# Optimization experiments

Measured on AMD Instinct MI355X. Metric: run time of the kernel, lower is better.

The kernel has to match this reference:

```python
import jax, jax.numpy as jnp
import numpy as np

B, T, F = 64, 96, 32          # batch, window_size, num_features
H_ENC, H_DEC = 128, 128       # encoder / decoder hidden sizes


def _lstm_cell(x, h, c, k, r, b):
    # Keras LSTMCell math: gates ordered i, f, g(candidate), o
    z = x @ k + h @ r + b
    i, f, g, o = jnp.split(z, 4, axis=-1)
    i = jax.nn.sigmoid(i)
    f = jax.nn.sigmoid(f)
    g = jnp.tanh(g)
    o = jax.nn.sigmoid(o)
    c_new = f * c + i * g
    h_new = o * jnp.tanh(c_new)
    return h_new, c_new


def setup_inputs() -> dict:
    key = jax.random.key(0)
    ks = jax.random.split(key, 20)
    s = 0.05
    d = {
        "inputs": jax.random.normal(ks[0], (B, T, F), jnp.float32),
        # encoder LSTMCell (input dim = F)
        "enc_k": jax.random.normal(ks[1], (F, 4 * H_ENC), jnp.float32) * s,
        "enc_r": jax.random.normal(ks[2], (H_ENC, 4 * H_ENC), jnp.float32) * s,
        "enc_b": jnp.zeros((4 * H_ENC,), jnp.float32),
        # encoder attention MLP: in = 2*H_ENC + T -> H_ENC -> 1
        "ae_w1": jax.random.normal(ks[3], (2 * H_ENC + T, H_ENC), jnp.float32) * s,
        "ae_b1": jnp.zeros((H_ENC,), jnp.float32),
        "ae_w2": jax.random.normal(ks[4], (H_ENC, 1), jnp.float32) * s,
        "ae_b2": jnp.zeros((1,), jnp.float32),
        # decoder LSTMCell (input dim = H_DEC, the fc output)
        "dec_k": jax.random.normal(ks[5], (H_DEC, 4 * H_DEC), jnp.float32) * s,
        "dec_r": jax.random.normal(ks[6], (H_DEC, 4 * H_DEC), jnp.float32) * s,
        "dec_b": jnp.zeros((4 * H_DEC,), jnp.float32),
        # decoder attention MLP: in = 2*H_DEC + H_ENC -> H_ENC -> 1
        "ad_w1": jax.random.normal(ks[7], (2 * H_DEC + H_ENC, H_ENC), jnp.float32) * s,
        "ad_b1": jnp.zeros((H_ENC,), jnp.float32),
        "ad_w2": jax.random.normal(ks[8], (H_ENC, 1), jnp.float32) * s,
        "ad_b2": jnp.zeros((1,), jnp.float32),
        # fc: (context H_ENC + y_prev 1) -> H_DEC
        "fc_w": jax.random.normal(ks[9], (H_ENC + 1, H_DEC), jnp.float32) * s,
        "fc_b": jnp.zeros((H_DEC,), jnp.float32),
        # fc_final: (d_n H_DEC + context H_ENC) -> F
        "ff_w": jax.random.normal(ks[10], (H_DEC + H_ENC, F), jnp.float32) * s,
        "ff_b": jnp.zeros((F,), jnp.float32),
    }
    return d


def reference(inputs, enc_k, enc_r, enc_b, ae_w1, ae_b1, ae_w2, ae_b2,
              dec_k, dec_r, dec_b, ad_w1, ad_b1, ad_w2, ad_b2,
              fc_w, fc_b, ff_w, ff_b):
    b, t, f = inputs.shape
    h_enc = enc_r.shape[0]
    h_dec = dec_r.shape[0]
    x_perm = jnp.transpose(inputs, (0, 2, 1))  # [B, F, T] (constant over time)

    # ---------------- encoder: input-attention LSTM over time ----------------
    def enc_step(carry, x_t):
        h, s = carry  # each [B, H_enc]
        hb = jnp.broadcast_to(h[:, None, :], (b, f, h_enc))
        sb = jnp.broadcast_to(s[:, None, :], (b, f, h_enc))
        cat = jnp.concatenate([hb, sb, x_perm], axis=2)       # [B, F, 2H+T]
        e = jnp.tanh(cat @ ae_w1 + ae_b1) @ ae_w2 + ae_b2     # [B, F, 1]
        alpha = jax.nn.softmax(e[..., 0], axis=1)             # [B, F]
        x_tilde = alpha * x_t                                 # [B, F]
        h, s = _lstm_cell(x_tilde, h, s, enc_k, enc_r, enc_b)
        return (h, s), h

    init = (jnp.zeros((b, h_enc), inputs.dtype), jnp.zeros((b, h_enc), inputs.dtype))
    _, h_all = jax.lax.scan(enc_step, init, jnp.transpose(inputs, (1, 0, 2)))
    x_encoded = jnp.transpose(h_all, (1, 0, 2))               # [B, T, H_enc]

    # ---------------- decoder: temporal-attention LSTM over time -------------
    y_prev = inputs[:, :, -1]                                 # [B, T]

    def dec_step(carry, y_t):
        d, c, _ = carry
        db = jnp.broadcast_to(d[:, None, :], (b, t, h_dec))
        cb = jnp.broadcast_to(c[:, None, :], (b, t, h_dec))
        cat = jnp.concatenate([db, cb, x_encoded], axis=2)    # [B, T, 2Hd+He]
        e = jnp.tanh(cat @ ad_w1 + ad_b1) @ ad_w2 + ad_b2     # [B, T, 1]
        beta = jax.nn.softmax(e[..., 0], axis=1)              # [B, T]
        ctx = jnp.einsum("bt,bth->bh", beta, x_encoded)       # [B, H_enc]
        y_tilde = jnp.concatenate([ctx, y_t[:, None]], axis=1) @ fc_w + fc_b
        d, c = _lstm_cell(y_tilde, d, c, dec_k, dec_r, dec_b)
        return (d, c, ctx), None

    init_d = (jnp.zeros((b, h_dec), inputs.dtype),
              jnp.zeros((b, h_dec), inputs.dtype),
              jnp.zeros((b, h_enc), inputs.dtype))
    (d_n, _, ctx), _ = jax.lax.scan(dec_step, init_d, jnp.transpose(y_prev, (1, 0)))

    y_pred = jnp.concatenate([d_n, ctx], axis=1) @ ff_w + ff_b  # [B, F]
    return y_pred[:, None, :]                                   # [B, 1, F]
```

## Files before the change

kernel.cpp:

```cpp
#include <hip/hip_runtime.h>

#define TT 96
#define FF 32
#define HH 128
#define G4 512
#define LOG2E 1.4426950408889634f

typedef _Float16 h2 __attribute__((ext_vector_type(2)));

__device__ __forceinline__ float fexp2(float x){ return __builtin_amdgcn_exp2f(x); }
__device__ __forceinline__ float frcp(float x){ return __builtin_amdgcn_rcpf(x); }
__device__ __forceinline__ float fsigmoid(float x){ return frcp(1.0f + fexp2(-LOG2E*x)); }
__device__ __forceinline__ float ftanh(float x){
    float u = fexp2(2.0f*LOG2E*x);
    return 1.0f - 2.0f*frcp(1.0f + u);
}
__device__ __forceinline__ h2 pk(float a, float b){
    h2 r; r.x = (_Float16)a; r.y = (_Float16)b; return r;
}
__device__ __forceinline__ unsigned pku(float a, float b){
    return __builtin_bit_cast(unsigned, pk(a, b));
}
__device__ __forceinline__ h2 u2h(unsigned v){ return __builtin_bit_cast(h2, v); }
__device__ __forceinline__ float fdot2(h2 a, h2 b, float c){
#if __has_builtin(__builtin_amdgcn_fdot2)
    return __builtin_amdgcn_fdot2(a, b, c, false);
#else
    return c + (float)a.x*(float)b.x + (float)a.y*(float)b.y;
#endif
}

__global__ __launch_bounds__(1024, 1)
void k_enc(const float* __restrict__ inputs,
           const float* __restrict__ enc_k,
           const float* __restrict__ enc_r,
           const float* __restrict__ enc_b,
           const float* __restrict__ ae_w1,
           const float* __restrict__ ae_b1,
           const float* __restrict__ ae_w2,
           const float* __restrict__ ad_w1,
           const float* __restrict__ fc_w,
           const float* __restrict__ fc_b,
           const float* __restrict__ dec_k,
           const float* __restrict__ dec_b,
           h2* __restrict__ Gp,
           float* __restrict__ gy,
           float* __restrict__ gb,
           float* __restrict__ ws_xenc,
           float* __restrict__ ws_xept){
    if (blockIdx.x >= 64){
        int blk = blockIdx.x - 64, tid = threadIdx.x;
        if (tid >= 256) return;
        int u0 = tid, u1 = tid + 256;
        if (blk < 16){
            float a0[8], a1[8];
            #pragma unroll
            for (int r = 0; r < 8; ++r){ a0[r] = 0.f; a1[r] = 0.f; }
            for (int m = 0; m < 128; ++m){
                float d0 = dec_k[m*G4 + u0], d1 = dec_k[m*G4 + u1];
                #pragma unroll
                for (int r = 0; r < 8; ++r){
                    float w = fc_w[(blk*8 + r)*HH + m];
                    a0[r] += w * d0; a1[r] += w * d1;
                }
            }
            #pragma unroll
            for (int c = 0; c < 4; ++c){
                Gp[(blk*G4 + u0)*4 + c] = pk(a0[2*c], a0[2*c+1]);
                Gp[(blk*G4 + u1)*4 + c] = pk(a1[2*c], a1[2*c+1]);
            }
        } else if (blk == 16){
            float a0 = 0.f, a1 = 0.f;
            for (int m = 0; m < 128; ++m){
                float w = fc_w[128*HH + m];
                a0 += w * dec_k[m*G4 + u0]; a1 += w * dec_k[m*G4 + u1];
            }
            gy[u0] = a0; gy[u1] = a1;
        } else {
            float a0 = 0.f, a1 = 0.f;
            for (int m = 0; m < 128; ++m){
                float w = fc_b[m];
                a0 += w * dec_k[m*G4 + u0]; a1 += w * dec_k[m*G4 + u1];
            }
            gb[u0] = a0 + dec_b[u0]; gb[u1] = a1 + dec_b[u1];
        }
        return;
    }

    extern __shared__ float lds[];
    uint4* KLH4 = (uint4*)lds;
    float* XPJT = lds + 8192;
    float* XIN  = lds + 12416;
    float* HST  = lds + 15488;
    float* PP   = lds + 15744;
    float* PPZ  = lds + 16768;
    float* PE   = lds + 17792;
    float* W2E  = lds + 17920;
    float* AB1E = lds + 18048;
    h2*    HSP  = (h2*)(lds + 18176);
    h2*    XTP  = (h2*)(lds + 18240);
    _Float16* XEF = (_Float16*)(lds + 18248);

    const int b = blockIdx.x, tid = threadIdx.x;
    const int u = tid & 511, hf = tid >> 9;
    const int j7 = tid & 127, g8 = tid >> 7;
    const float* xin_g = inputs + b*TT*FF;

    for (int i = tid; i < TT*FF; i += 1024) XIN[i] = xin_g[i];
    for (int i = tid; i < 2048; i += 1024){
        int f8 = i >> 9, uu = i & 511;
        uint4 q;
        q.x = pku(enc_k[(f8*8+0)*G4+uu], enc_k[(f8*8+1)*G4+uu]);
        q.y = pku(enc_k[(f8*8+2)*G4+uu], enc_k[(f8*8+3)*G4+uu]);
        q.z = pku(enc_k[(f8*8+4)*G4+uu], enc_k[(f8*8+5)*G4+uu]);
        q.w = pku(enc_k[(f8*8+6)*G4+uu], enc_k[(f8*8+7)*G4+uu]);
        KLH4[i] = q;
    }
    if (tid < 128){ W2E[tid] = ae_w2[tid]; AB1E[tid] = ae_b1[tid]; HSP[tid] = pk(0.f, 0.f); }
    if (tid < 256) HST[tid] = 0.f;

    h2 rp_e[32];
    #pragma unroll
    for (int i = 0; i < 32; ++i)
        rp_e[i] = pk(enc_r[(hf*64 + 2*i)*G4 + u], enc_r[(hf*64 + 2*i+1)*G4 + u]);

    uint4 wae[4];
    #pragma unroll
    for (int i4 = 0; i4 < 4; ++i4){
        int r0 = (g8*4 + i4)*8;
        wae[i4].x = pku(ae_w1[(r0+0)*HH + j7], ae_w1[(r0+1)*HH + j7]);
        wae[i4].y = pku(ae_w1[(r0+2)*HH + j7], ae_w1[(r0+3)*HH + j7]);
        wae[i4].z = pku(ae_w1[(r0+4)*HH + j7], ae_w1[(r0+5)*HH + j7]);
        wae[i4].w = pku(ae_w1[(r0+6)*HH + j7], ae_w1[(r0+7)*HH + j7]);
    }

    const float eb = (hf == 0) ? enc_b[u] : 0.f;
    __syncthreads();

    {
        int j = tid & 127, fh = tid >> 7;
        float a0=0.f, a1=0.f, a2=0.f, a3=0.f;
        for (int t = 0; t < TT; ++t){
            float w = ae_w1[(256 + t)*HH + j];
            const float* xr = &XIN[t*FF + fh*4];
            a0 += xr[0]*w; a1 += xr[1]*w; a2 += xr[2]*w; a3 += xr[3]*w;
        }
        XPJT[j*33 + fh*4 + 0] = a0;
        XPJT[j*33 + fh*4 + 1] = a1;
        XPJT[j*33 + fh*4 + 2] = a2;
        XPJT[j*33 + fh*4 + 3] = a3;
    }
    __syncthreads();

    const int f5 = tid & 31, jg5 = tid >> 5;
    float er_e[4], sumw2e = 0.f;
    #pragma unroll
    for (int i = 0; i < 4; ++i){
        er_e[i] = fexp2(2.0f*LOG2E * XPJT[(jg5*4 + i)*33 + f5]);
        sumw2e += W2E[jg5*4 + i];
    }

    const uint4* HSP4 = (const uint4*)HSP;
    const uint4* XTP4 = (const uint4*)XTP;

    for (int t = 0; t < TT; ++t){
        float z = eb;
        {
            float a0 = 0.f, a1 = 0.f;
            #pragma unroll
            for (int i4 = 0; i4 < 4; ++i4){
                uint4 q  = HSP4[g8*4 + i4];
                uint4 wv = wae[i4];
                a0 = fdot2(u2h(q.x), u2h(wv.x), a0);
                a1 = fdot2(u2h(q.y), u2h(wv.y), a1);
                a0 = fdot2(u2h(q.z), u2h(wv.z), a0);
                a1 = fdot2(u2h(q.w), u2h(wv.w), a1);
            }
            PP[tid] = a0 + a1;
        }
        if (tid < 128){
            float z2 = 0.f;
            #pragma unroll
            for (int i4 = 0; i4 < 8; ++i4){
                uint4 q = HSP4[hf*8 + i4];
                z  = fdot2(u2h(q.x), rp_e[i4*4+0], z);
                z2 = fdot2(u2h(q.y), rp_e[i4*4+1], z2);
                z  = fdot2(u2h(q.z), rp_e[i4*4+2], z);
                z2 = fdot2(u2h(q.w), rp_e[i4*4+3], z2);
            }
            z += z2;
        }
        __syncthreads();
        if (tid < 128){
            float s = AB1E[tid];
            #pragma unroll
            for (int g = 0; g < 8; ++g) s += PP[tid + 128*g];
            PE[tid] = fexp2(2.0f*LOG2E * s);
        } else {
            float z2 = 0.f;
            #pragma unroll
            for (int i4 = 0; i4 < 8; ++i4){
                uint4 q = HSP4[hf*8 + i4];
                z  = fdot2(u2h(q.x), rp_e[i4*4+0], z);
                z2 = fdot2(u2h(q.y), rp_e[i4*4+1], z2);
                z  = fdot2(u2h(q.z), rp_e[i4*4+2], z);
                z2 = fdot2(u2h(q.w), rp_e[i4*4+3], z2);
            }
            z += z2;
        }
        __syncthreads();
        {
            float acc2 = 0.f;
            #pragma unroll
            for (int i = 0; i < 4; ++i){
                float uu = PE[jg5*4 + i];
                float w  = W2E[jg5*4 + i];
                acc2 += w * frcp(fmaf(er_e[i], uu, 1.0f));
            }
            PP[tid] = sumw2e - 2.0f*acc2;
        }
        __syncthreads();
        if (tid < 64){
            int f = tid & 31, hh = tid >> 5;
            float e = 0.f;
            #pragma unroll
            for (int g = 0; g < 16; ++g) e += PP[(hh*16 + g)*32 + f];
            e += __shfl_xor(e, 32, 64);
            float p = fexp2(e * LOG2E);
            float ss = p;
            #pragma unroll
            for (int d = 16; d; d >>= 1) ss += __shfl_xor(ss, d, 32);
            if (tid < 32){
                float xt = p * frcp(ss) * XIN[t*FF + tid];
                float xt2 = __shfl_xor(xt, 1);
                if (!(tid & 1)) XTP[tid >> 1] = pk(xt, xt2);
            }
        }
        __syncthreads();
        {
            float z2 = 0.f;
            #pragma unroll
            for (int c = 0; c < 2; ++c){
                int f8 = hf*2 + c;
                uint4 kq = KLH4[f8*512 + u];
                uint4 xq = XTP4[f8];
                z  = fdot2(u2h(kq.x), u2h(xq.x), z);
                z2 = fdot2(u2h(kq.y), u2h(xq.y), z2);
                z  = fdot2(u2h(kq.z), u2h(xq.z), z);
                z2 = fdot2(u2h(kq.w), u2h(xq.w), z2);
            }
            PPZ[hf*512 + u] = z + z2;
        }
        __syncthreads();
        if (tid < 128){
            int j = tid;
            float zi = PPZ[j]       + PPZ[512 + j];
            float zf = PPZ[128 + j] + PPZ[640 + j];
            float zg = PPZ[256 + j] + PPZ[768 + j];
            float zo = PPZ[384 + j] + PPZ[896 + j];
            float iv = fsigmoid(zi);
            float fv = fsigmoid(zf);
            float gv = ftanh(zg);
            float ov = fsigmoid(zo);
            float cn = fv * HST[128 + j] + iv * gv;
            float hn = ov * ftanh(cn);
            HST[128 + j] = cn;
            HST[j] = hn;
            ws_xenc[(b*TT + t)*HH + j] = hn;
            XEF[t*HH + j] = (_Float16)hn;
            float hn2 = __shfl_xor(hn, 1);
            float cn2 = __shfl_xor(cn, 1);
            if (!(j & 1)){
                HSP[j >> 1]        = pk(hn, hn2);
                HSP[64 + (j >> 1)] = pk(cn, cn2);
            }
        }
        __syncthreads();
    }

    {
        int j = tid & 127, th = tid >> 7;
        float acc[12];
        #pragma unroll
        for (int i = 0; i < 12; ++i) acc[i] = 0.f;
        for (int k = 0; k < 128; ++k){
            float w = ad_w1[(256 + k)*HH + j];
            #pragma unroll
            for (int i = 0; i < 12; ++i)
                acc[i] += (float)XEF[(th*12 + i)*HH + k] * w;
        }
        #pragma unroll
        for (int i = 0; i < 12; ++i)
            ws_xept[(b*HH + j)*TT + th*12 + i] = acc[i];
    }
}

__global__ __launch_bounds__(1024, 1)
void k_dec(const float* __restrict__ inputs,
           const float* __restrict__ dec_r,
           const float* __restrict__ ad_w1,
           const float* __restrict__ ad_b1,
           const float* __restrict__ ad_w2,
           const float* __restrict__ ff_w,
           const float* __restrict__ ff_b,
           const h2* __restrict__ Gp,
           const float* __restrict__ gy,
           const float* __restrict__ gb,
           const float* __restrict__ ws_xenc,
           const float* __restrict__ ws_xept,
           float* __restrict__ out){
    extern __shared__ float lds[];
    uint4* XE4 = (uint4*)lds;
    uint4* WDC4= (uint4*)(lds + 6144);
    float* PP  = lds + 22528;
    float* PPZ = lds + 23552;
    float* PPA = lds + 24576;
    float* APJP= lds + 25600;
    float* DST = lds + 25760;
    float* CTX = lds + 26016;
    float* WSUM= lds + 26144;
    float* YV  = lds + 26160;
    h2*    DCP = (h2*)(lds + 26256);
    h2*    CXP = (h2*)(lds + 26384);
    h2*    BEP = (h2*)(lds + 26448);

    const int b = blockIdx.x, tid = threadIdx.x;
    const int u = tid & 511, hf = tid >> 9;
    const int j = tid & 127, og = tid >> 7;

    {
        const float* xe_g = ws_xenc + b*TT*HH;
        for (int i = tid; i < 12*HH; i += 1024){
            int t8 = i >> 7, k = i & 127;
            uint4 qq;
            qq.x = pku(xe_g[(t8*8 + 0)*HH + k], xe_g[(t8*8 + 1)*HH + k]);
            qq.y = pku(xe_g[(t8*8 + 2)*HH + k], xe_g[(t8*8 + 3)*HH + k]);
            qq.z = pku(xe_g[(t8*8 + 4)*HH + k], xe_g[(t8*8 + 5)*HH + k]);
            qq.w = pku(xe_g[(t8*8 + 6)*HH + k], xe_g[(t8*8 + 7)*HH + k]);
            XE4[i] = qq;
        }
    }
    for (int i = tid; i < 4096; i += 1024){
        int jj = i & 127, i4g = i >> 7;
        int kbase = (i4g >> 2)*32 + (i4g & 3)*8;
        uint4 wv;
        wv.x = pku(ad_w1[(kbase+0)*HH + jj], ad_w1[(kbase+1)*HH + jj]);
        wv.y = pku(ad_w1[(kbase+2)*HH + jj], ad_w1[(kbase+3)*HH + jj]);
        wv.z = pku(ad_w1[(kbase+4)*HH + jj], ad_w1[(kbase+5)*HH + jj]);
        wv.w = pku(ad_w1[(kbase+6)*HH + jj], ad_w1[(kbase+7)*HH + jj]);
        WDC4[i] = wv;
    }
    if (tid < TT) YV[tid] = inputs[b*TT*FF + tid*FF + (FF-1)];
    if (tid < 128) DCP[tid] = pk(0.f, 0.f);
    if (tid < 256) DST[tid] = 0.f;

    h2 rp[32];
    #pragma unroll
    for (int i = 0; i < 32; ++i)
        rp[i] = pk(dec_r[(hf*64 + 2*i)*G4 + u], dec_r[(hf*64 + 2*i+1)*G4 + u]);

    uint4 Greg[8];
    {
        const uint4* GQ = (const uint4*)Gp;
        #pragma unroll
        for (int g = 0; g < 8; ++g) Greg[g] = GQ[(hf*8 + g)*G4 + u];
    }

    const int l6 = tid & 63, wv6 = tid >> 6;
    const int ogn = l6 & 7, tpl = l6 >> 3;
    const int tpn = wv6*6 + tpl;
    const bool act = (tpl < 6);
    float erw[16], iw[16], sumw2 = 0.f;
    {
        const float* xp_g = ws_xept + (b*HH + ogn*16)*TT + tpn;
        #pragma unroll
        for (int i = 0; i < 16; ++i){
            float w2v = ad_w2[ogn*16 + i];
            float ivv = 1.0f / w2v;
            iw[i] = ivv;
            sumw2 += w2v;
            float xp = act ? xp_g[i*TT] : 0.f;
            erw[i] = fexp2(2.0f*LOG2E * xp) * ivv;
        }
    }

    const float gbr = gb[u], gyr = gy[u];
    const float ab1 = (tid < 128) ? ad_b1[tid] : 0.f;
    __syncthreads();

    const uint4* DCP4 = (const uint4*)DCP;
    const uint4* CXP4 = (const uint4*)CXP;
    const uint4* BEP4 = (const uint4*)BEP;

    for (int t = 0; t < TT; ++t){
        float z = (hf == 0) ? (gbr + YV[t]*gyr) : 0.f;
        {
            float s0 = 0.f, s1 = 0.f;
            #pragma unroll
            for (int i = 0; i < 4; ++i){
                uint4 dq = DCP4[og*4 + i];
                uint4 wv = WDC4[(og*4 + i)*128 + j];
                s0 = fdot2(u2h(dq.x), u2h(wv.x), s0);
                s1 = fdot2(u2h(dq.y), u2h(wv.y), s1);
                s0 = fdot2(u2h(dq.z), u2h(wv.z), s0);
                s1 = fdot2(u2h(dq.w), u2h(wv.w), s1);
            }
            PPA[og*128 + j] = s0 + s1;
        }
        if (tid < 128){
            float z2 = 0.f;
            #pragma unroll
            for (int i4 = 0; i4 < 8; ++i4){
                uint4 q = DCP4[hf*8 + i4];
                z  = fdot2(u2h(q.x), rp[i4*4+0], z);
                z2 = fdot2(u2h(q.y), rp[i4*4+1], z2);
                z  = fdot2(u2h(q.z), rp[i4*4+2], z);
                z2 = fdot2(u2h(q.w), rp[i4*4+3], z2);
            }
            z += z2;
        }
        __syncthreads();
        if (tid < 128){
            float s = ab1;
            #pragma unroll
            for (int g = 0; g < 8; ++g) s += PPA[tid + 128*g];
            APJP[(tid >> 4)*20 + (tid & 15)] = fexp2(2.0f*LOG2E * s);
        } else {
            float z2 = 0.f;
            #pragma unroll
            for (int i4 = 0; i4 < 8; ++i4){
                uint4 q = DCP4[hf*8 + i4];
                z  = fdot2(u2h(q.x), rp[i4*4+0], z);
                z2 = fdot2(u2h(q.y), rp[i4*4+1], z2);
                z  = fdot2(u2h(q.z), rp[i4*4+2], z);
                z2 = fdot2(u2h(q.w), rp[i4*4+3], z2);
            }
            z += z2;
        }
        __syncthreads();
        {
            float part = 0.f;
            if (act){
                float acc2 = 0.f;
                #pragma unroll
                for (int q4 = 0; q4 < 4; ++q4){
                    float4 uj = *(const float4*)&APJP[ogn*20 + q4*4];
                    acc2 += frcp(fmaf(erw[q4*4+0], uj.x, iw[q4*4+0]));
                    acc2 += frcp(fmaf(erw[q4*4+1], uj.y, iw[q4*4+1]));
                    acc2 += frcp(fmaf(erw[q4*4+2], uj.z, iw[q4*4+2]));
                    acc2 += frcp(fmaf(erw[q4*4+3], uj.w, iw[q4*4+3]));
                }
                part = sumw2 - 2.0f*acc2;
            }
            part += __shfl_xor(part, 1);
            part += __shfl_xor(part, 2);
            part += __shfl_xor(part, 4);
            float p = fexp2(part * LOG2E);
            float p2 = __shfl_xor(p, 8);
            if (act && ogn == 0 && !(tpl & 1))
                BEP[wv6*3 + (tpl >> 1)] = pk(p, p2);
            float pss = (act && ogn == 0) ? p : 0.f;
            pss += __shfl_xor(pss, 8);
            pss += __shfl_xor(pss, 16);
            pss += __shfl_xor(pss, 32);
            if (l6 == 0) WSUM[wv6] = pss;
        }
        __syncthreads();
        if (tid < 128){
            float ssn = 0.f;
            #pragma unroll
            for (int g = 0; g < 16; ++g) ssn += WSUM[g];
            float rs = frcp(ssn);
            float s0 = 0.f, s1 = 0.f;
            #pragma unroll
            for (int t8 = 0; t8 < 12; t8 += 2){
                uint4 xq0 = XE4[t8*HH + tid],     bb0 = BEP4[t8];
                uint4 xq1 = XE4[(t8+1)*HH + tid], bb1 = BEP4[t8+1];
                s0 = fdot2(u2h(xq0.x), u2h(bb0.x), s0);
                s1 = fdot2(u2h(xq0.y), u2h(bb0.y), s1);
                s0 = fdot2(u2h(xq0.z), u2h(bb0.z), s0);
                s1 = fdot2(u2h(xq0.w), u2h(bb0.w), s1);
                s0 = fdot2(u2h(xq1.x), u2h(bb1.x), s0);
                s1 = fdot2(u2h(xq1.y), u2h(bb1.y), s1);
                s0 = fdot2(u2h(xq1.z), u2h(bb1.z), s0);
                s1 = fdot2(u2h(xq1.w), u2h(bb1.w), s1);
            }
            float cv = (s0 + s1) * rs;
            CTX[tid] = cv;
            float cv2 = __shfl_xor(cv, 1);
            if (!(tid & 1)) CXP[tid >> 1] = pk(cv, cv2);
        }
        __syncthreads();
        {
            float z2 = 0.f;
            #pragma unroll
            for (int gi = 0; gi < 8; ++gi){
                uint4 q  = Greg[gi];
                uint4 cc = CXP4[hf*8 + gi];
                z  = fdot2(u2h(q.x), u2h(cc.x), z);
                z2 = fdot2(u2h(q.y), u2h(cc.y), z2);
                z  = fdot2(u2h(q.z), u2h(cc.z), z);
                z2 = fdot2(u2h(q.w), u2h(cc.w), z2);
            }
            PPZ[hf*512 + u] = z + z2;
        }
        __syncthreads();
        if (tid < 128){
            int jj = tid;
            float zi = PPZ[jj]       + PPZ[512 + jj];
            float zf = PPZ[128 + jj] + PPZ[640 + jj];
            float zg = PPZ[256 + jj] + PPZ[768 + jj];
            float zo = PPZ[384 + jj] + PPZ[896 + jj];
            float iv = fsigmoid(zi);
            float fv = fsigmoid(zf);
            float gv = ftanh(zg);
            float ov = fsigmoid(zo);
            float cn = fv * DST[128 + jj] + iv * gv;
            float hn = ov * ftanh(cn);
            DST[128 + jj] = cn;
            DST[jj] = hn;
            float hn2 = __shfl_xor(hn, 1);
            float cn2 = __shfl_xor(cn, 1);
            if (!(jj & 1)){
                DCP[jj >> 1]        = pk(hn, hn2);
                DCP[64 + (jj >> 1)] = pk(cn, cn2);
            }
        }
        __syncthreads();
    }

    {
        int jp = tid & 31, sg = tid >> 5;
        float a = 0.f;
        #pragma unroll
        for (int kk = 0; kk < 8; ++kk){
            int k = sg*8 + kk;
            float val = (k < 128) ? DST[k] : CTX[k - 128];
            a += val * ff_w[k*FF + jp];
        }
        PP[sg*32 + jp] = a;
    }
    __syncthreads();
    if (tid < 32){
        float o = ff_b[tid];
        #pragma unroll
        for (int s = 0; s < 32; ++s) o += PP[s*32 + tid];
        out[b*FF + tid] = o;
    }
}

extern "C" void kernel_launch(void* const* d_in, const int* in_sizes, int n_in,
                              void* d_out, int out_size, void* d_ws, size_t ws_size,
                              hipStream_t stream) {
    const float* inputs = (const float*)d_in[0];
    const float* enc_k  = (const float*)d_in[1];
    const float* enc_r  = (const float*)d_in[2];
    const float* enc_b  = (const float*)d_in[3];
    const float* ae_w1  = (const float*)d_in[4];
    const float* ae_b1  = (const float*)d_in[5];
    const float* ae_w2  = (const float*)d_in[6];
    const float* dec_k  = (const float*)d_in[8];
    const float* dec_r  = (const float*)d_in[9];
    const float* dec_b  = (const float*)d_in[10];
    const float* ad_w1  = (const float*)d_in[11];
    const float* ad_b1  = (const float*)d_in[12];
    const float* ad_w2  = (const float*)d_in[13];
    const float* fc_w   = (const float*)d_in[15];
    const float* fc_b   = (const float*)d_in[16];
    const float* ff_w   = (const float*)d_in[17];
    const float* ff_b   = (const float*)d_in[18];

    float* ws      = (float*)d_ws;
    float* ws_xenc = ws;
    float* ws_xept = ws + 786432;
    h2*    Gp      = (h2*)(ws + 1572864);
    float* gy      = ws + 1605632;
    float* gb      = ws + 1606144;

    hipFuncSetAttribute((const void*)k_enc, hipFuncAttributeMaxDynamicSharedMemorySize, 97568);
    hipFuncSetAttribute((const void*)k_dec, hipFuncAttributeMaxDynamicSharedMemorySize, 106048);

    k_enc<<<82, 1024, 97568, stream>>>(inputs, enc_k, enc_r, enc_b, ae_w1, ae_b1, ae_w2,
                                       ad_w1, fc_w, fc_b, dec_k, dec_b, Gp, gy, gb,
                                       ws_xenc, ws_xept);
    k_dec<<<64, 1024, 106048, stream>>>(inputs, dec_r, ad_w1, ad_b1, ad_w2, ff_w, ff_b,
                                        Gp, gy, gb, ws_xenc, ws_xept, (float*)d_out);
}
```

Measured before the change: 652.1 us.

## Remap decoder gate columns per lane and finish the LSTM cell with wave shuffles

Decoder threads are reassigned so that each group of 8 lanes holds the i, f, g and o gate columns (both K-halves) for one hidden unit. The two half-sums are combined with xor-shuffles and the gates are gathered with intra-wave shuffles. This removes the PPZ LDS buffer and one __syncthreads per time step, and the cell state now lives in a register. All threads run the gate activations redundantly, and the strided column mapping may change the global access pattern for the dec_r and Gp preloads.

```diff
diff --git a/kernel.cpp b/kernel.cpp
--- a/kernel.cpp
+++ b/kernel.cpp
@@ -313,20 +313,22 @@
     uint4* XE4 = (uint4*)lds;
     uint4* WDC4= (uint4*)(lds + 6144);
     float* PP  = lds + 22528;
-    float* PPZ = lds + 23552;
-    float* PPA = lds + 24576;
-    float* APJP= lds + 25600;
-    float* DST = lds + 25760;
-    float* CTX = lds + 26016;
-    float* WSUM= lds + 26144;
-    float* YV  = lds + 26160;
-    h2*    DCP = (h2*)(lds + 26256);
-    h2*    CXP = (h2*)(lds + 26384);
-    h2*    BEP = (h2*)(lds + 26448);
+    float* PPA = lds + 23552;
+    float* APJP= lds + 24576;
+    float* DST = lds + 24736;
+    float* CTX = lds + 24864;
+    float* WSUM= lds + 24992;
+    float* YV  = lds + 25008;
+    h2*    DCP = (h2*)(lds + 25104);
+    h2*    CXP = (h2*)(lds + 25232);
+    h2*    BEP = (h2*)(lds + 25296);
 
     const int b = blockIdx.x, tid = threadIdx.x;
-    const int u = tid & 511, hf = tid >> 9;
     const int j = tid & 127, og = tid >> 7;
+    const int hfn = tid & 1, v = tid >> 1;
+    const int jd = v >> 2, gate = v & 3;
+    const int colidx = gate*128 + jd;
+    const int l6d = tid & 63;
 
     {
         const float* xe_g = ws_xenc + b*TT*HH;
@@ -352,22 +354,21 @@
     }
     if (tid < TT) YV[tid] = inputs[b*TT*FF + tid*FF + (FF-1)];
     if (tid < 128) DCP[tid] = pk(0.f, 0.f);
-    if (tid < 256) DST[tid] = 0.f;
 
     h2 rp[32];
     #pragma unroll
     for (int i = 0; i < 32; ++i)
-        rp[i] = pk(dec_r[(hf*64 + 2*i)*G4 + u], dec_r[(hf*64 + 2*i+1)*G4 + u]);
+        rp[i] = pk(dec_r[(hfn*64 + 2*i)*G4 + colidx], dec_r[(hfn*64 + 2*i+1)*G4 + colidx]);
 
     uint4 Greg[8];
     {
         const uint4* GQ = (const uint4*)Gp;
         #pragma unroll
-        for (int g = 0; g < 8; ++g) Greg[g] = GQ[(hf*8 + g)*G4 + u];
-    }
-
-    const int l6 = tid & 63, wv6 = tid >> 6;
-    const int ogn = l6 & 7, tpl = l6 >> 3;
+        for (int g = 0; g < 8; ++g) Greg[g] = GQ[(hfn*8 + g)*G4 + colidx];
+    }
+
+    const int wv6 = tid >> 6;
+    const int ogn = l6d & 7, tpl = l6d >> 3;
     const int tpn = wv6*6 + tpl;
     const bool act = (tpl < 6);
     float erw[16], iw[16], sumw2 = 0.f;
@@ -384,8 +385,9 @@
         }
     }
 
-    const float gbr = gb[u], gyr = gy[u];
+    const float gbr = gb[colidx], gyr = gy[colidx];
     const float ab1 = (tid < 128) ? ad_b1[tid] : 0.f;
+    float creg = 0.f;
     __syncthreads();
 
     const uint4* DCP4 = (const uint4*)DCP;
@@ -393,7 +395,7 @@
     const uint4* BEP4 = (const uint4*)BEP;
 
     for (int t = 0; t < TT; ++t){
-        float z = (hf == 0) ? (gbr + YV[t]*gyr) : 0.f;
+        float z = (hfn == 0) ? (gbr + YV[t]*gyr) : 0.f;
         {
             float s0 = 0.f, s1 = 0.f;
             #pragma unroll
@@ -411,7 +413,7 @@
             float z2 = 0.f;
             #pragma unroll
             for (int i4 = 0; i4 < 8; ++i4){
-                uint4 q = DCP4[hf*8 + i4];
+                uint4 q = DCP4[hfn*8 + i4];
                 z  = fdot2(u2h(q.x), rp[i4*4+0], z);
                 z2 = fdot2(u2h(q.y), rp[i4*4+1], z2);
                 z  = fdot2(u2h(q.z), rp[i4*4+2], z);
@@ -429,7 +431,7 @@
             float z2 = 0.f;
             #pragma unroll
             for (int i4 = 0; i4 < 8; ++i4){
-                uint4 q = DCP4[hf*8 + i4];
+                uint4 q = DCP4[hfn*8 + i4];
                 z  = fdot2(u2h(q.x), rp[i4*4+0], z);
                 z2 = fdot2(u2h(q.y), rp[i4*4+1], z2);
                 z  = fdot2(u2h(q.z), rp[i4*4+2], z);
@@ -463,7 +465,7 @@
             pss += __shfl_xor(pss, 8);
             pss += __shfl_xor(pss, 16);
             pss += __shfl_xor(pss, 32);
-            if (l6 == 0) WSUM[wv6] = pss;
+            if (l6d == 0) WSUM[wv6] = pss;
         }
         __syncthreads();
         if (tid < 128){
@@ -496,34 +498,29 @@
             #pragma unroll
             for (int gi = 0; gi < 8; ++gi){
                 uint4 q  = Greg[gi];
-                uint4 cc = CXP4[hf*8 + gi];
+                uint4 cc = CXP4[hfn*8 + gi];
                 z  = fdot2(u2h(q.x), u2h(cc.x), z);
                 z2 = fdot2(u2h(q.y), u2h(cc.y), z2);
                 z  = fdot2(u2h(q.z), u2h(cc.z), z);
                 z2 = fdot2(u2h(q.w), u2h(cc.w), z2);
             }
-            PPZ[hf*512 + u] = z + z2;
-        }
-        __syncthreads();
-        if (tid < 128){
-            int jj = tid;
-            float zi = PPZ[jj]       + PPZ[512 + jj];
-            float zf = PPZ[128 + jj] + PPZ[640 + jj];
-            float zg = PPZ[256 + jj] + PPZ[768 + jj];
-            float zo = PPZ[384 + jj] + PPZ[896 + jj];
-            float iv = fsigmoid(zi);
-            float fv = fsigmoid(zf);
-            float gv = ftanh(zg);
-            float ov = fsigmoid(zo);
-            float cn = fv * DST[128 + jj] + iv * gv;
+            z += z2;
+            float zfull = z + __shfl_xor(z, 1);
+            float a = (gate == 2) ? ftanh(zfull) : fsigmoid(zfull);
+            int base = l6d & ~7;
+            float iv = __shfl(a, base + 0, 64);
+            float fv = __shfl(a, base + 2, 64);
+            float gv = __shfl(a, base + 4, 64);
+            float ov = __shfl(a, base + 6, 64);
+            float cn = fv * creg + iv * gv;
             float hn = ov * ftanh(cn);
-            DST[128 + jj] = cn;
-            DST[jj] = hn;
-            float hn2 = __shfl_xor(hn, 1);
-            float cn2 = __shfl_xor(cn, 1);
-            if (!(jj & 1)){
-                DCP[jj >> 1]        = pk(hn, hn2);
-                DCP[64 + (jj >> 1)] = pk(cn, cn2);
+            creg = cn;
+            if ((l6d & 7) == 0) DST[jd] = hn;
+            float hnB = __shfl(hn, (l6d + 8) & 63, 64);
+            float cnB = __shfl(cn, (l6d + 8) & 63, 64);
+            if ((l6d & 15) == 0){
+                DCP[jd >> 1]        = pk(hn, hnB);
+                DCP[64 + (jd >> 1)] = pk(cn, cnB);
             }
         }
         __syncthreads();
@@ -578,11 +575,11 @@
     float* gb      = ws + 1606144;
 
     hipFuncSetAttribute((const void*)k_enc, hipFuncAttributeMaxDynamicSharedMemorySize, 97568);
-    hipFuncSetAttribute((const void*)k_dec, hipFuncAttributeMaxDynamicSharedMemorySize, 106048);
+    hipFuncSetAttribute((const void*)k_dec, hipFuncAttributeMaxDynamicSharedMemorySize, 101440);
 
     k_enc<<<82, 1024, 97568, stream>>>(inputs, enc_k, enc_r, enc_b, ae_w1, ae_b1, ae_w2,
                                        ad_w1, fc_w, fc_b, dec_k, dec_b, Gp, gy, gb,
                                        ws_xenc, ws_xept);
-    k_dec<<<64, 1024, 106048, stream>>>(inputs, dec_r, ad_w1, ad_b1, ad_w2, ff_w, ff_b,
+    k_dec<<<64, 1024, 101440, stream>>>(inputs, dec_r, ad_w1, ad_b1, ad_w2, ff_w, ff_b,
                                         Gp, gy, gb, ws_xenc, ws_xept, (float*)d_out);
 }
```

Result: slower. 672.3 us (+3.1%).
